# Performance work log

Hardware: AMD Instinct MI355X
Metric: run time of the kernel (lower is better)

Reference implementation:

```python
import jax, jax.numpy as jnp
import numpy as np

BETA = 0.25  # commitment weight


def setup_inputs() -> dict:
    key = jax.random.key(0)
    k1, k2 = jax.random.split(key)
    B, N, D, K = 16, 1024, 512, 8192
    z_e = jax.random.normal(k1, (B, N, D), dtype=jnp.float32)
    # codebook weight; torch init is uniform(-1/K, 1/K), scale doesn't affect math structure
    W = jax.random.uniform(k2, (K, D), dtype=jnp.float32, minval=-1.0 / K, maxval=1.0 / K)
    return {"z_e": z_e, "W": W}


def reference(z_e, W):
    B, N, D = z_e.shape
    flat = z_e.reshape(B * N, D)
    dist = (jnp.sum(flat * flat, axis=1, keepdims=True)
            + jnp.sum(W * W, axis=1)[None, :]
            - 2.0 * (flat @ W.T))
    ids = jnp.argmin(dist, axis=1)           # [B*N]
    z_q = W[ids].reshape(B, N, D)            # embedding gather
    codebook_loss = jnp.mean((z_q - jax.lax.stop_gradient(z_e)) ** 2)
    commit_loss = jnp.mean((z_e - jax.lax.stop_gradient(z_q)) ** 2)
    vq_loss = codebook_loss + BETA * commit_loss
    orth_loss = jnp.zeros((), dtype=z_e.dtype)  # orth_reg_weight == 0.0
    loss_total = vq_loss + 0.0 * orth_loss
    z_q_st = z_e + jax.lax.stop_gradient(z_q - z_e)  # straight-through
    return (z_q_st, ids.reshape(B, N), vq_loss, codebook_loss, commit_loss, orth_loss, loss_total)
```

## Files before the change

kernel.cpp:

```cpp
#include <hip/hip_runtime.h>
#include <math.h>

#define MROWS 16384
#define DIMD  512
#define KCOD  8192
#define CAP   2097152u
#define MARGIN_S 17.0f

typedef __attribute__((ext_vector_type(4))) float f32x4;
typedef const __attribute__((address_space(1))) unsigned char glb_byte;
typedef __attribute__((address_space(3))) unsigned char lds_byte;

__device__ __forceinline__ void gload16(const void* g, void* l) {
    __builtin_amdgcn_global_load_lds((glb_byte*)g, (lds_byte*)l, 16, 0, 0);
}

__device__ __forceinline__ unsigned f2e4m3(float f) {
    const unsigned b = __float_as_uint(f);
    const unsigned s = (b >> 24) & 0x80u;
    const unsigned ef = (b >> 23) & 0xFFu;
    const unsigned m = b & 0x7FFFFFu;
    if (ef == 0u) return s;
    const int e = (int)ef - 127;
    if (e >= -6) {
        unsigned q = m >> 20;
        const unsigned rem = m & 0xFFFFFu;
        q += (rem > 0x80000u) || (rem == 0x80000u && (q & 1u));
        unsigned te = (unsigned)(e + 7);
        if (q == 8u) { q = 0u; te += 1u; }
        if (te > 15u || (te == 15u && q == 7u)) return s | 0x7Eu;
        return s | (te << 3) | q;
    } else {
        const int sh = 20 + (-6 - e);
        if (sh > 31) return s;
        const unsigned m24 = 0x800000u | m;
        unsigned q = m24 >> sh;
        const unsigned rem = m24 & ((1u << sh) - 1u);
        const unsigned hlf = 1u << (sh - 1);
        q += (rem > hlf) || (rem == hlf && (q & 1u));
        if (q == 8u) return s | 0x08u;
        return s | q;
    }
}

#define OFF_A8      0u
#define OFF_W8T     8388608u
#define OFF_XSQ     12582912u
#define OFF_WSQ     12648448u
#define OFF_THR     12681216u
#define OFF_PM2     12746752u
#define OFF_RES     21135360u
#define OFF_CTCNT   21266432u
#define OFF_GCNT    21266688u
#define OFF_CTROWS  21266944u
#define OFF_LIST    23364096u
#define OFF_PARTIAL 31752704u
#define OFF_IDX     31818240u

__global__ __launch_bounds__(256) void cvt2_k(const float* __restrict__ A,
                                              const float* __restrict__ W,
                                              unsigned char* __restrict__ A8,
                                              unsigned char* __restrict__ W8T,
                                              float* __restrict__ xsq,
                                              float* __restrict__ wsq,
                                              unsigned int* __restrict__ ctcnt,
                                              unsigned int* __restrict__ gcount)
{
    if (blockIdx.x == 0 && threadIdx.x < 65) {
        if (threadIdx.x < 64) ctcnt[threadIdx.x] = 0u;
        else *gcount = 0u;
    }
    const int lane = threadIdx.x & 63;
    const int wid  = (blockIdx.x * blockDim.x + threadIdx.x) >> 6;
    const int nw   = (gridDim.x * blockDim.x) >> 6;
    for (int r = wid; r < MROWS + KCOD; r += nw) {
        const bool isA = (r < MROWS);
        const float4* src = (const float4*)(isA ? (A + (size_t)r * DIMD)
                                                : (W + (size_t)(r - MROWS) * DIMD));
        float4 v0 = src[lane];
        float4 v1 = src[lane + 64];
        float s = v0.x*v0.x + v0.y*v0.y + v0.z*v0.z + v0.w*v0.w
                + v1.x*v1.x + v1.y*v1.y + v1.z*v1.z + v1.w*v1.w;
        #pragma unroll
        for (int m = 1; m < 64; m <<= 1) s += __shfl_xor(s, m, 64);
        if (lane == 0) { if (isA) xsq[r] = s; else wsq[r - MROWS] = s; }

        if (isA) {
            const unsigned p0 = f2e4m3(v0.x) | (f2e4m3(v0.y) << 8) | (f2e4m3(v0.z) << 16) | (f2e4m3(v0.w) << 24);
            const unsigned p1 = f2e4m3(v1.x) | (f2e4m3(v1.y) << 8) | (f2e4m3(v1.z) << 16) | (f2e4m3(v1.w) << 24);
            *(unsigned*)(A8 + (size_t)r * DIMD + 4 * lane) = p0;
            *(unsigned*)(A8 + (size_t)r * DIMD + 256 + 4 * lane) = p1;
        } else {
            const int rw = r - MROWS;
            const int CT = rw >> 7, code = rw & 127;
            const unsigned p0 = f2e4m3(v0.x*8192.f) | (f2e4m3(v0.y*8192.f) << 8) | (f2e4m3(v0.z*8192.f) << 16) | (f2e4m3(v0.w*8192.f) << 24);
            const unsigned p1 = f2e4m3(v1.x*8192.f) | (f2e4m3(v1.y*8192.f) << 8) | (f2e4m3(v1.z*8192.f) << 16) | (f2e4m3(v1.w*8192.f) << 24);
            const size_t basea = (size_t)CT * 65536 + (size_t)(code >> 6) * 2048
                               + (size_t)((lane >> 1) & 3) * 512
                               + (size_t)(code & 63) * 8 + 4 * (lane & 1);
            *(unsigned*)(W8T + basea + (size_t)(lane >> 3) * 4096) = p0;
            *(unsigned*)(W8T + basea + (size_t)(8 + (lane >> 3)) * 4096) = p1;
        }
    }
}

__global__ __launch_bounds__(128, 2) void minpass_k(
    const unsigned char* __restrict__ A8,
    const unsigned char* __restrict__ W8T,
    float* __restrict__ partmin2)
{
    __shared__ __align__(16) unsigned char Bs[2][6][2048];
    __shared__ __align__(16) float pm[64 * 32];
    __shared__ __align__(16) unsigned char dmy[2048];

    const int t    = threadIdx.x;
    const int lane = t & 63;
    const int wv   = t >> 6;
    const int rt   = (int)blockIdx.x & 255;
    const int q    = (int)blockIdx.x >> 8;
    const int r0   = rt * 64;

    long Areg[16][4];
    {
        const unsigned char* ab = A8 + (size_t)(r0 + (lane & 15)) * DIMD + (lane >> 4) * 8;
        #pragma unroll
        for (int kc = 0; kc < 16; ++kc)
            #pragma unroll
            for (int mi = 0; mi < 4; ++mi)
                Areg[kc][mi] = *(const long*)(ab + (size_t)mi * 16 * DIMD + kc * 32);
    }

    const unsigned char* Wq = W8T + (size_t)q * 1048576 + wv * 2048;

    #pragma unroll
    for (int c = 0; c < 4; ++c) {
        const unsigned char* s = Wq + c * 4096 + lane * 16;
        gload16(s,        &Bs[wv][c][lane * 16]);
        gload16(s + 1024, &Bs[wv][c][1024 + lane * 16]);
    }
    int pfs = 4, rds = 0;

    f32x4 acc[4][4];
    #pragma unroll
    for (int mi = 0; mi < 4; ++mi)
        #pragma unroll
        for (int ni = 0; ni < 4; ++ni) acc[mi][ni] = (f32x4){0.f, 0.f, 0.f, 0.f};

    for (int ct = 0; ct < 16; ++ct) {
        #pragma unroll
        for (int kc = 0; kc < 16; ++kc) {
            const int n = ct * 16 + kc + 4;
            if (n < 256) {
                const unsigned char* s = Wq + n * 4096 + lane * 16;
                gload16(s,        &Bs[wv][pfs][lane * 16]);
                gload16(s + 1024, &Bs[wv][pfs][1024 + lane * 16]);
            } else {
                gload16(Wq + lane * 16, &dmy[t * 16]);
                gload16(Wq + lane * 16, &dmy[t * 16]);
            }
            pfs = (pfs == 5) ? 0 : pfs + 1;

            asm volatile("s_waitcnt vmcnt(8)" ::: "memory");

            const unsigned char* bb = &Bs[wv][rds][0];
            long b[4];
            #pragma unroll
            for (int ni = 0; ni < 4; ++ni)
                b[ni] = *(const long*)(bb + (lane >> 4) * 512 + (ni * 16 + (lane & 15)) * 8);
            #pragma unroll
            for (int mi = 0; mi < 4; ++mi)
                #pragma unroll
                for (int ni = 0; ni < 4; ++ni)
                    acc[mi][ni] = __builtin_amdgcn_mfma_f32_16x16x32_fp8_fp8(Areg[kc][mi], b[ni], acc[mi][ni], 0, 0, 0);
            rds = (rds == 5) ? 0 : rds + 1;
        }

        #pragma unroll
        for (int mi = 0; mi < 4; ++mi) {
            #pragma unroll
            for (int reg = 0; reg < 4; ++reg) {
                float mx = fmaxf(fmaxf(acc[mi][0][reg], acc[mi][1][reg]),
                                 fmaxf(acc[mi][2][reg], acc[mi][3][reg]));
                #pragma unroll
                for (int s = 1; s < 16; s <<= 1) mx = fmaxf(mx, __shfl_xor(mx, s, 64));
                if ((lane & 15) == 0)
                    pm[(mi * 16 + (lane >> 4) * 4 + reg) * 32 + ct * 2 + wv] = -2.0f * mx;
                acc[mi][0][reg] = 0.f; acc[mi][1][reg] = 0.f;
                acc[mi][2][reg] = 0.f; acc[mi][3][reg] = 0.f;
            }
        }
    }

    __syncthreads();
    const int row = t >> 1, ch = (t & 1) * 16;
    #pragma unroll
    for (int j = 0; j < 4; ++j) {
        f32x4 v = *(const f32x4*)&pm[row * 32 + ch + j * 4];
        *(f32x4*)&partmin2[(size_t)(r0 + row) * 128 + q * 32 + ch + j * 4] = v;
    }
}

__global__ __launch_bounds__(256) void qualify_k(const float* __restrict__ partmin2,
                                                 float* __restrict__ rowthr,
                                                 unsigned int* __restrict__ ctcnt,
                                                 unsigned short* __restrict__ ctrows,
                                                 unsigned long long* __restrict__ res)
{
    __shared__ unsigned cntA[64], baseL[64], cntB[64];
    const int t = threadIdx.x;
    const int r = blockIdx.x * 256 + t;

    if (t < 64) { cntA[t] = 0u; cntB[t] = 0u; }

    const f32x4* p = (const f32x4*)(partmin2 + (size_t)r * 128);
    float m = INFINITY;
    for (int i = 0; i < 32; ++i) {
        f32x4 x = p[i];
        m = fminf(fminf(fminf(x[0], x[1]), fminf(x[2], x[3])), m);
    }
    const float thr = m + MARGIN_S;
    rowthr[r] = thr;
    res[r] = ~0ull;

    unsigned long long qm = 0ull;
    for (int i = 0; i < 32; ++i) {
        f32x4 x = p[i];
        if (fminf(x[0], x[1]) <= thr) qm |= 1ull << (2 * i);
        if (fminf(x[2], x[3]) <= thr) qm |= 1ull << (2 * i + 1);
    }
    __syncthreads();
    unsigned long long mm = qm;
    while (mm) {
        const int tile = __ffsll((long long)mm) - 1;
        mm &= mm - 1;
        atomicAdd(&cntA[tile], 1u);
    }
    __syncthreads();
    if (t < 64) baseL[t] = cntA[t] ? atomicAdd(&ctcnt[t], cntA[t]) : 0u;
    __syncthreads();
    mm = qm;
    while (mm) {
        const int tile = __ffsll((long long)mm) - 1;
        mm &= mm - 1;
        const unsigned pos = baseL[tile] + atomicAdd(&cntB[tile], 1u);
        ctrows[tile * 16384 + pos] = (unsigned short)r;
    }
}

__global__ __launch_bounds__(256) void cand_k(
    const unsigned char* __restrict__ A8,
    const unsigned char* __restrict__ W8T,
    const float* __restrict__ rowthr,
    const unsigned int* __restrict__ ctcnt,
    const unsigned short* __restrict__ ctrows,
    unsigned int* __restrict__ list,
    unsigned int* __restrict__ gcount)
{
    __shared__ __align__(16) unsigned char As[2][4096];
    __shared__ __align__(16) unsigned char Bs[2][4096];
    __shared__ int ids_lds[128];
    __shared__ float thr_lds[128];
    __shared__ unsigned wtot[4];
    __shared__ unsigned gb_lds;

    const int T = blockIdx.x;
    unsigned n = ctcnt[T]; if (n > 16384u) n = 16384u;
    const unsigned base = blockIdx.y * 128;
    if (base >= n) return;

    const int t    = threadIdx.x;
    const int lane = t & 63;
    const int w    = t >> 6;
    const int wm   = w >> 1, wn = w & 1;
    const int c0   = T * 128;

    if (t < 128) {
        const int g = (base + t < n) ? (int)ctrows[T * 16384 + base + t] : -1;
        ids_lds[t] = (g < 0) ? 0 : g;
        thr_lds[t] = (g < 0) ? -INFINITY : rowthr[g];
    }
    __syncthreads();

    const unsigned char* bbase = W8T + (size_t)T * 65536;
    const int srow = t >> 1, skh = (t & 1) * 16;

    gload16(A8 + (size_t)ids_lds[srow] * DIMD + skh, &As[0][t * 16]);
    gload16(bbase + t * 16, &Bs[0][t * 16]);

    f32x4 acc[4][4];
    #pragma unroll
    for (int mi = 0; mi < 4; ++mi)
        #pragma unroll
        for (int ni = 0; ni < 4; ++ni) acc[mi][ni] = (f32x4){0.f, 0.f, 0.f, 0.f};

    int cur = 0;
    for (int kc = 0; kc < 16; ++kc) {
        __syncthreads();
        if (kc + 1 < 16) {
            const int nb = cur ^ 1;
            gload16(A8 + (size_t)ids_lds[srow] * DIMD + (kc + 1) * 32 + skh, &As[nb][t * 16]);
            gload16(bbase + (kc + 1) * 4096 + t * 16, &Bs[nb][t * 16]);
        }
        long a[4], b[4];
        #pragma unroll
        for (int mi = 0; mi < 4; ++mi)
            a[mi] = *(const long*)&As[cur][(wm * 64 + mi * 16 + (lane & 15)) * 32 + (lane >> 4) * 8];
        #pragma unroll
        for (int ni = 0; ni < 4; ++ni)
            b[ni] = *(const long*)&Bs[cur][wn * 2048 + (lane >> 4) * 512 + (ni * 16 + (lane & 15)) * 8];
        #pragma unroll
        for (int mi = 0; mi < 4; ++mi)
            #pragma unroll
            for (int ni = 0; ni < 4; ++ni)
                acc[mi][ni] = __builtin_amdgcn_mfma_f32_16x16x32_fp8_fp8(a[mi], b[ni], acc[mi][ni], 0, 0, 0);
        __syncthreads();
        cur ^= 1;
    }

    unsigned nh = 0;
    #pragma unroll
    for (int mi = 0; mi < 4; ++mi)
        #pragma unroll
        for (int reg = 0; reg < 4; ++reg) {
            const float thr = thr_lds[wm * 64 + mi * 16 + (lane >> 4) * 4 + reg];
            #pragma unroll
            for (int ni = 0; ni < 4; ++ni)
                if (-2.0f * acc[mi][ni][reg] <= thr) ++nh;
        }

    unsigned pfx = nh;
    #pragma unroll
    for (int s = 1; s < 64; s <<= 1) {
        unsigned v = __shfl_up(pfx, s, 64);
        if (lane >= s) pfx += v;
    }
    if (lane == 63) wtot[w] = pfx;
    __syncthreads();
    if (t == 0) {
        const unsigned tot = wtot[0] + wtot[1] + wtot[2] + wtot[3];
        gb_lds = tot ? atomicAdd(gcount, tot) : 0u;
    }
    __syncthreads();
    unsigned wb = 0;
    #pragma unroll
    for (int i = 0; i < 4; ++i) if (i < w) wb += wtot[i];
    unsigned myoff = gb_lds + wb + pfx - nh;

    #pragma unroll
    for (int mi = 0; mi < 4; ++mi)
        #pragma unroll
        for (int reg = 0; reg < 4; ++reg) {
            const int row_l = wm * 64 + mi * 16 + (lane >> 4) * 4 + reg;
            const float thr = thr_lds[row_l];
            #pragma unroll
            for (int ni = 0; ni < 4; ++ni) {
                if (-2.0f * acc[mi][ni][reg] <= thr) {
                    const unsigned k = c0 + wn * 64 + ni * 16 + (lane & 15);
                    if (myoff < CAP)
                        list[myoff] = ((unsigned)ids_lds[row_l] << 13) | k;
                    ++myoff;
                }
            }
        }
}

__global__ __launch_bounds__(256) void refine_k(const float* __restrict__ A,
                                                const float* __restrict__ W,
                                                const float* __restrict__ xsq,
                                                const float* __restrict__ wsq,
                                                const unsigned* __restrict__ list,
                                                const unsigned* __restrict__ gcount,
                                                unsigned long long* __restrict__ res)
{
    const int gl  = threadIdx.x & 15;
    const int gid = (blockIdx.x * 256 + threadIdx.x) >> 4;
    const int ngr = (gridDim.x * 256) >> 4;
    unsigned n = *gcount;
    if (n > CAP) n = CAP;
    for (unsigned i = gid; i < n; i += ngr) {
        const unsigned pk = list[i];
        const unsigned row = pk >> 13, k = pk & 8191u;
        const float4* xp = (const float4*)(A + (size_t)row * DIMD);
        const float4* wp = (const float4*)(W + (size_t)k * DIMD);
        double s = 0.0;
        #pragma unroll
        for (int j = 0; j < 8; ++j) {
            const float4 x = xp[j * 16 + gl];
            const float4 w = wp[j * 16 + gl];
            s += (double)x.x * w.x + (double)x.y * w.y
               + (double)x.z * w.z + (double)x.w * w.w;
        }
        #pragma unroll
        for (int m = 1; m < 16; m <<= 1) s += __shfl_xor(s, m, 64);
        if (gl == 0) {
            const float Df = (float)s;
            const float dist = (xsq[row] + wsq[k]) - 2.0f * Df;
            const unsigned long long p =
                ((unsigned long long)__float_as_uint(dist) << 32) | (unsigned long long)k;
            atomicMin(res + row, p);
        }
    }
}

__global__ __launch_bounds__(256) void finish_k(const unsigned long long* __restrict__ res,
                                                int* __restrict__ idxo,
                                                float* __restrict__ out_ids)
{
    const int r = blockIdx.x * 256 + threadIdx.x;
    const int id = (int)(res[r] & 8191ull);
    idxo[r] = id;
    out_ids[r] = (float)id;
}

__global__ __launch_bounds__(256) void gather_k(const float* __restrict__ A,
                                                const float* __restrict__ W,
                                                const int* __restrict__ idx,
                                                float* __restrict__ out_zq,
                                                double* __restrict__ partial)
{
    __shared__ double wsum[4];
    const int t   = threadIdx.x;
    const int row = blockIdx.x * 2 + (t >> 7);
    const int col = t & 127;
    const int id  = idx[row];
    const float4 ze = ((const float4*)(A + (size_t)row * DIMD))[col];
    const float4 zq = ((const float4*)(W + (size_t)id  * DIMD))[col];
    float4 o;
    o.x = ze.x + (zq.x - ze.x);
    o.y = ze.y + (zq.y - ze.y);
    o.z = ze.z + (zq.z - ze.z);
    o.w = ze.w + (zq.w - ze.w);
    ((float4*)(out_zq + (size_t)row * DIMD))[col] = o;
    const float dx = zq.x - ze.x, dy = zq.y - ze.y, dz = zq.z - ze.z, dw = zq.w - ze.w;
    double s = (double)dx*dx + (double)dy*dy + (double)dz*dz + (double)dw*dw;
    #pragma unroll
    for (int m = 1; m < 64; m <<= 1) s += __shfl_xor(s, m, 64);
    if ((t & 63) == 0) wsum[t >> 6] = s;
    __syncthreads();
    if (t == 0) partial[blockIdx.x] = (wsum[0] + wsum[1]) + (wsum[2] + wsum[3]);
}

__global__ __launch_bounds__(256) void fin_k(const double* __restrict__ partial,
                                             float* __restrict__ outs)
{
    __shared__ double wsum[4];
    const int t = threadIdx.x;
    double s = 0.0;
    for (int i = 0; i < 32; ++i) s += partial[t + 256 * i];
    #pragma unroll
    for (int m = 1; m < 64; m <<= 1) s += __shfl_xor(s, m, 64);
    if ((t & 63) == 0) wsum[t >> 6] = s;
    __syncthreads();
    if (t == 0) {
        const double tot = (wsum[0] + wsum[1]) + (wsum[2] + wsum[3]);
        const double mse = tot / (double)((size_t)MROWS * DIMD);
        const float mf = (float)mse;
        const float vq = (float)(mse * 1.25);
        outs[0] = vq; outs[1] = mf; outs[2] = mf; outs[3] = 0.0f; outs[4] = vq;
    }
}


extern "C" void kernel_launch(void* const* d_in, const int* in_sizes, int n_in,
                              void* d_out, int out_size, void* d_ws, size_t ws_size,
                              hipStream_t stream)
{
    const float* A = (const float*)d_in[0];
    const float* W = (const float*)d_in[1];

    char* ws = (char*)d_ws;
    unsigned char* A8  = (unsigned char*)(ws + OFF_A8);
    unsigned char* W8T = (unsigned char*)(ws + OFF_W8T);
    float*  xsq     = (float*)(ws + OFF_XSQ);
    float*  wsq     = (float*)(ws + OFF_WSQ);
    float*  rowthr  = (float*)(ws + OFF_THR);
    float*  partmin2= (float*)(ws + OFF_PM2);
    unsigned long long* res = (unsigned long long*)(ws + OFF_RES);
    unsigned int* ctcnt     = (unsigned int*)(ws + OFF_CTCNT);
    unsigned int* gcount    = (unsigned int*)(ws + OFF_GCNT);
    unsigned short* ctrows  = (unsigned short*)(ws + OFF_CTROWS);
    unsigned int* list      = (unsigned int*)(ws + OFF_LIST);
    double* partial = (double*)(ws + OFF_PARTIAL);
    int*    idx     = (int*)(ws + OFF_IDX);

    float* out_zq  = (float*)d_out;
    float* out_ids = out_zq + (size_t)MROWS * DIMD;
    float* out_sc  = out_ids + MROWS;

    cvt2_k<<<512, 256, 0, stream>>>(A, W, A8, W8T, xsq, wsq, ctcnt, gcount);
    minpass_k<<<1024, 128, 0, stream>>>(A8, W8T, partmin2);
    qualify_k<<<64, 256, 0, stream>>>(partmin2, rowthr, ctcnt, ctrows, res);
    cand_k<<<dim3(64, 128), 256, 0, stream>>>(A8, W8T, rowthr, ctcnt, ctrows, list, gcount);
    refine_k<<<512, 256, 0, stream>>>(A, W, xsq, wsq, list, gcount, res);
    finish_k<<<64, 256, 0, stream>>>(res, idx, out_ids);
    gather_k<<<8192, 256, 0, stream>>>(A, W, idx, out_zq, partial);
    fin_k<<<1, 256, 0, stream>>>(partial, out_sc);
}
```

Before: 340.5 us.

## Restructure fp8 min-pass tiling with shared B buffers and fuse finish into gather

```diff
diff --git a/kernel.cpp b/kernel.cpp
--- a/kernel.cpp
+++ b/kernel.cpp
@@ -55,7 +55,6 @@
 #define OFF_CTROWS  21266944u
 #define OFF_LIST    23364096u
 #define OFF_PARTIAL 31752704u
-#define OFF_IDX     31818240u
 
 __global__ __launch_bounds__(256) void cvt2_k(const float* __restrict__ A,
                                               const float* __restrict__ W,
@@ -92,111 +91,106 @@
             *(unsigned*)(A8 + (size_t)r * DIMD + 256 + 4 * lane) = p1;
         } else {
             const int rw = r - MROWS;
-            const int CT = rw >> 7, code = rw & 127;
+            const int CT = rw >> 7, half = (rw >> 6) & 1, c6 = rw & 63;
             const unsigned p0 = f2e4m3(v0.x*8192.f) | (f2e4m3(v0.y*8192.f) << 8) | (f2e4m3(v0.z*8192.f) << 16) | (f2e4m3(v0.w*8192.f) << 24);
             const unsigned p1 = f2e4m3(v1.x*8192.f) | (f2e4m3(v1.y*8192.f) << 8) | (f2e4m3(v1.z*8192.f) << 16) | (f2e4m3(v1.w*8192.f) << 24);
-            const size_t basea = (size_t)CT * 65536 + (size_t)(code >> 6) * 2048
+            const size_t basea = (size_t)CT * 65536 + (size_t)half * 32768
                                + (size_t)((lane >> 1) & 3) * 512
-                               + (size_t)(code & 63) * 8 + 4 * (lane & 1);
-            *(unsigned*)(W8T + basea + (size_t)(lane >> 3) * 4096) = p0;
-            *(unsigned*)(W8T + basea + (size_t)(8 + (lane >> 3)) * 4096) = p1;
-        }
-    }
-}
-
-__global__ __launch_bounds__(128, 2) void minpass_k(
+                               + (size_t)c6 * 8 + 4 * (lane & 1);
+            *(unsigned*)(W8T + basea + (size_t)(lane >> 3) * 2048) = p0;
+            *(unsigned*)(W8T + basea + (size_t)(8 + (lane >> 3)) * 2048) = p1;
+        }
+    }
+}
+
+__global__ __launch_bounds__(256, 4) void minpass_k(
     const unsigned char* __restrict__ A8,
     const unsigned char* __restrict__ W8T,
     float* __restrict__ partmin2)
 {
-    __shared__ __align__(16) unsigned char Bs[2][6][2048];
-    __shared__ __align__(16) float pm[64 * 32];
-    __shared__ __align__(16) unsigned char dmy[2048];
+    __shared__ __align__(16) unsigned char Bs[8][2048];
+    __shared__ __align__(16) unsigned char dmy[1024];
 
     const int t    = threadIdx.x;
     const int lane = t & 63;
     const int wv   = t >> 6;
-    const int rt   = (int)blockIdx.x & 255;
-    const int q    = (int)blockIdx.x >> 8;
-    const int r0   = rt * 64;
-
-    long Areg[16][4];
+    const int rt   = (int)blockIdx.x & 127;
+    const int q    = (int)blockIdx.x >> 7;
+    const int r0   = rt * 128;
+
+    long Areg[16][2];
     {
-        const unsigned char* ab = A8 + (size_t)(r0 + (lane & 15)) * DIMD + (lane >> 4) * 8;
-        #pragma unroll
-        for (int kc = 0; kc < 16; ++kc)
-            #pragma unroll
-            for (int mi = 0; mi < 4; ++mi)
-                Areg[kc][mi] = *(const long*)(ab + (size_t)mi * 16 * DIMD + kc * 32);
-    }
-
-    const unsigned char* Wq = W8T + (size_t)q * 1048576 + wv * 2048;
-
-    #pragma unroll
-    for (int c = 0; c < 4; ++c) {
-        const unsigned char* s = Wq + c * 4096 + lane * 16;
-        gload16(s,        &Bs[wv][c][lane * 16]);
-        gload16(s + 1024, &Bs[wv][c][1024 + lane * 16]);
-    }
-    int pfs = 4, rds = 0;
-
-    f32x4 acc[4][4];
-    #pragma unroll
-    for (int mi = 0; mi < 4; ++mi)
-        #pragma unroll
-        for (int ni = 0; ni < 4; ++ni) acc[mi][ni] = (f32x4){0.f, 0.f, 0.f, 0.f};
-
-    for (int ct = 0; ct < 16; ++ct) {
+        const unsigned char* ab = A8 + (size_t)(r0 + wv * 32 + (lane & 15)) * DIMD + (lane >> 4) * 8;
         #pragma unroll
         for (int kc = 0; kc < 16; ++kc) {
-            const int n = ct * 16 + kc + 4;
-            if (n < 256) {
-                const unsigned char* s = Wq + n * 4096 + lane * 16;
-                gload16(s,        &Bs[wv][pfs][lane * 16]);
-                gload16(s + 1024, &Bs[wv][pfs][1024 + lane * 16]);
-            } else {
-                gload16(Wq + lane * 16, &dmy[t * 16]);
-                gload16(Wq + lane * 16, &dmy[t * 16]);
+            Areg[kc][0] = *(const long*)(ab + kc * 32);
+            Areg[kc][1] = *(const long*)(ab + (size_t)16 * DIMD + kc * 32);
+        }
+    }
+
+    const unsigned char* Wq = W8T + (size_t)q * 524288;
+
+    {
+        const unsigned char* s = Wq + wv * 2048 + lane * 16;
+        gload16(s,        &Bs[wv][lane * 16]);
+        gload16(s + 1024, &Bs[wv][1024 + lane * 16]);
+    }
+
+    const int qd = lane >> 4, c15 = lane & 15;
+    const int pair = lane & 7;
+    const int erow = r0 + wv * 32 + (pair >> 2) * 16 + qd * 4 + (pair & 3);
+    float* const estore = partmin2 + (size_t)erow * 128 + q * 16;
+
+    for (int g = 0; g < 16; ++g) {
+        f32x4 acc[2][4];
+        #pragma unroll
+        for (int mi = 0; mi < 2; ++mi)
+            #pragma unroll
+            for (int ni = 0; ni < 4; ++ni) acc[mi][ni] = (f32x4){0.f, 0.f, 0.f, 0.f};
+
+        #pragma unroll
+        for (int kc = 0; kc < 16; ++kc) {
+            const int n = g * 16 + kc;
+            if ((kc & 3) == wv) {
+                const int np = n + 4;
+                if (np < 256) {
+                    const unsigned char* s = Wq + (size_t)np * 2048 + lane * 16;
+                    gload16(s,        &Bs[np & 7][lane * 16]);
+                    gload16(s + 1024, &Bs[np & 7][1024 + lane * 16]);
+                } else {
+                    gload16(Wq + lane * 16, &dmy[lane * 16]);
+                    gload16(Wq + lane * 16, &dmy[lane * 16]);
+                }
+                asm volatile("s_waitcnt vmcnt(2)" ::: "memory");
             }
-            pfs = (pfs == 5) ? 0 : pfs + 1;
-
-            asm volatile("s_waitcnt vmcnt(8)" ::: "memory");
-
-            const unsigned char* bb = &Bs[wv][rds][0];
+            __builtin_amdgcn_s_barrier();
+            __builtin_amdgcn_sched_barrier(0);
+
+            const unsigned char* bb = &Bs[n & 7][qd * 512 + c15 * 8];
             long b[4];
             #pragma unroll
             for (int ni = 0; ni < 4; ++ni)
-                b[ni] = *(const long*)(bb + (lane >> 4) * 512 + (ni * 16 + (lane & 15)) * 8);
-            #pragma unroll
-            for (int mi = 0; mi < 4; ++mi)
+                b[ni] = *(const long*)(bb + ni * 128);
+            #pragma unroll
+            for (int mi = 0; mi < 2; ++mi)
                 #pragma unroll
                 for (int ni = 0; ni < 4; ++ni)
                     acc[mi][ni] = __builtin_amdgcn_mfma_f32_16x16x32_fp8_fp8(Areg[kc][mi], b[ni], acc[mi][ni], 0, 0, 0);
-            rds = (rds == 5) ? 0 : rds + 1;
-        }
-
-        #pragma unroll
-        for (int mi = 0; mi < 4; ++mi) {
+        }
+
+        float keep = 0.f;
+        #pragma unroll
+        for (int mi = 0; mi < 2; ++mi) {
             #pragma unroll
             for (int reg = 0; reg < 4; ++reg) {
                 float mx = fmaxf(fmaxf(acc[mi][0][reg], acc[mi][1][reg]),
                                  fmaxf(acc[mi][2][reg], acc[mi][3][reg]));
                 #pragma unroll
                 for (int s = 1; s < 16; s <<= 1) mx = fmaxf(mx, __shfl_xor(mx, s, 64));
-                if ((lane & 15) == 0)
-                    pm[(mi * 16 + (lane >> 4) * 4 + reg) * 32 + ct * 2 + wv] = -2.0f * mx;
-                acc[mi][0][reg] = 0.f; acc[mi][1][reg] = 0.f;
-                acc[mi][2][reg] = 0.f; acc[mi][3][reg] = 0.f;
+                if (pair == mi * 4 + reg) keep = mx;
             }
         }
-    }
-
-    __syncthreads();
-    const int row = t >> 1, ch = (t & 1) * 16;
-    #pragma unroll
-    for (int j = 0; j < 4; ++j) {
-        f32x4 v = *(const f32x4*)&pm[row * 32 + ch + j * 4];
-        *(f32x4*)&partmin2[(size_t)(r0 + row) * 128 + q * 32 + ch + j * 4] = v;
+        estore[g] = -2.0f * keep;
     }
 }
 
@@ -283,9 +277,10 @@
 
     const unsigned char* bbase = W8T + (size_t)T * 65536;
     const int srow = t >> 1, skh = (t & 1) * 16;
+    const int bh = t >> 7, bt = t & 127;
 
     gload16(A8 + (size_t)ids_lds[srow] * DIMD + skh, &As[0][t * 16]);
-    gload16(bbase + t * 16, &Bs[0][t * 16]);
+    gload16(bbase + (size_t)bh * 32768 + bt * 16, &Bs[0][t * 16]);
 
     f32x4 acc[4][4];
     #pragma unroll
@@ -299,7 +294,7 @@
         if (kc + 1 < 16) {
             const int nb = cur ^ 1;
             gload16(A8 + (size_t)ids_lds[srow] * DIMD + (kc + 1) * 32 + skh, &As[nb][t * 16]);
-            gload16(bbase + (kc + 1) * 4096 + t * 16, &Bs[nb][t * 16]);
+            gload16(bbase + (size_t)bh * 32768 + (kc + 1) * 2048 + bt * 16, &Bs[nb][t * 16]);
         }
         long a[4], b[4];
         #pragma unroll
@@ -402,27 +397,19 @@
     }
 }
 
-__global__ __launch_bounds__(256) void finish_k(const unsigned long long* __restrict__ res,
-                                                int* __restrict__ idxo,
-                                                float* __restrict__ out_ids)
-{
-    const int r = blockIdx.x * 256 + threadIdx.x;
-    const int id = (int)(res[r] & 8191ull);
-    idxo[r] = id;
-    out_ids[r] = (float)id;
-}
-
 __global__ __launch_bounds__(256) void gather_k(const float* __restrict__ A,
                                                 const float* __restrict__ W,
-                                                const int* __restrict__ idx,
+                                                const unsigned long long* __restrict__ res,
                                                 float* __restrict__ out_zq,
+                                                float* __restrict__ out_ids,
                                                 double* __restrict__ partial)
 {
     __shared__ double wsum[4];
     const int t   = threadIdx.x;
     const int row = blockIdx.x * 2 + (t >> 7);
     const int col = t & 127;
-    const int id  = idx[row];
+    const int id  = (int)(res[row] & 8191ull);
+    if ((t & 127) == 0) out_ids[row] = (float)id;
     const float4 ze = ((const float4*)(A + (size_t)row * DIMD))[col];
     const float4 zq = ((const float4*)(W + (size_t)id  * DIMD))[col];
     float4 o;
@@ -481,18 +468,16 @@
     unsigned short* ctrows  = (unsigned short*)(ws + OFF_CTROWS);
     unsigned int* list      = (unsigned int*)(ws + OFF_LIST);
     double* partial = (double*)(ws + OFF_PARTIAL);
-    int*    idx     = (int*)(ws + OFF_IDX);
 
     float* out_zq  = (float*)d_out;
     float* out_ids = out_zq + (size_t)MROWS * DIMD;
     float* out_sc  = out_ids + MROWS;
 
     cvt2_k<<<512, 256, 0, stream>>>(A, W, A8, W8T, xsq, wsq, ctcnt, gcount);
-    minpass_k<<<1024, 128, 0, stream>>>(A8, W8T, partmin2);
+    minpass_k<<<1024, 256, 0, stream>>>(A8, W8T, partmin2);
     qualify_k<<<64, 256, 0, stream>>>(partmin2, rowthr, ctcnt, ctrows, res);
     cand_k<<<dim3(64, 128), 256, 0, stream>>>(A8, W8T, rowthr, ctcnt, ctrows, list, gcount);
-    refine_k<<<512, 256, 0, stream>>>(A, W, xsq, wsq, list, gcount, res);
-    finish_k<<<64, 256, 0, stream>>>(res, idx, out_ids);
-    gather_k<<<8192, 256, 0, stream>>>(A, W, idx, out_zq, partial);
+    refine_k<<<1024, 256, 0, stream>>>(A, W, xsq, wsq, list, gcount, res);
+    gather_k<<<8192, 256, 0, stream>>>(A, W, res, out_zq, out_ids, partial);
     fin_k<<<1, 256, 0, stream>>>(partial, out_sc);
 }
```

Result: faster. 289.9 us (-14.9%).
